# Performance work log

Hardware: AMD Instinct MI355X
Metric: run time of the kernel (lower is better)

Reference implementation:

```python
import jax, jax.numpy as jnp
import numpy as np

NEG = -1e30  # stand-in for -inf that keeps logaddexp grad-safe


def _ctc_neg_log_likelihood(predictions, labels):
    # predictions: [B, T, C] logits; labels: [B, L] int, -1 = padding.
    # tf.nn.ctc_loss(blank_index=-1) => blank class is C-1.
    B, T, C = predictions.shape
    L = labels.shape[1]
    S = 2 * L + 1
    blank = C - 1

    label_len = jnp.sum((labels != -1).astype(jnp.int32), axis=-1)  # [B]
    labels_c = jnp.where(labels < 0, 0, labels).astype(jnp.int32)

    # Extended label sequence: blank, l1, blank, l2, ..., blank  -> [B, S]
    ext = jnp.full((B, S), blank, dtype=jnp.int32)
    ext = ext.at[:, 1::2].set(labels_c)

    # s-2 transition allowed only at label positions (odd s) with ext[s] != ext[s-2]
    same = jnp.concatenate([jnp.zeros((B, 2), bool), ext[:, 2:] == ext[:, :-2]], axis=1)
    is_label_pos = (jnp.arange(S) % 2 == 1)[None, :]
    allow2 = is_label_pos & ~same  # [B, S]

    # valid extended positions per example: s < 2*label_len + 1
    valid = jnp.arange(S)[None, :] < (2 * label_len + 1)[:, None]  # [B, S]

    log_probs = jax.nn.log_softmax(predictions, axis=-1)  # [B, T, C]
    # emission log-prob for each extended-label slot: [B, T, S]
    lp_ext = jnp.take_along_axis(log_probs, jnp.broadcast_to(ext[:, None, :], (B, T, S)), axis=2)

    has_lab = label_len > 0
    alpha0 = jnp.full((B, S), NEG, dtype=log_probs.dtype)
    alpha0 = alpha0.at[:, 0].set(lp_ext[:, 0, 0])
    alpha0 = alpha0.at[:, 1].set(jnp.where(has_lab, lp_ext[:, 0, 1], NEG))
    alpha0 = jnp.where(valid, alpha0, NEG)

    def step(alpha, lp_t):
        a1 = alpha
        a2 = jnp.pad(alpha, ((0, 0), (1, 0)), constant_values=NEG)[:, :S]
        a3 = jnp.pad(alpha, ((0, 0), (2, 0)), constant_values=NEG)[:, :S]
        a3 = jnp.where(allow2, a3, NEG)
        new = jnp.logaddexp(jnp.logaddexp(a1, a2), a3) + lp_t
        new = jnp.where(valid, new, NEG)
        return new, None

    lp_rest = jnp.moveaxis(lp_ext[:, 1:], 1, 0)  # [T-1, B, S]
    alphaT, _ = jax.lax.scan(step, alpha0, lp_rest)

    idx1 = (2 * label_len)[:, None]              # final blank
    idx2 = jnp.maximum(idx1 - 1, 0)              # final label
    a_end1 = jnp.take_along_axis(alphaT, idx1, axis=1)[:, 0]
    a_end2 = jnp.take_along_axis(alphaT, idx2, axis=1)[:, 0]
    a_end2 = jnp.where(has_lab, a_end2, NEG)
    log_lik = jnp.logaddexp(a_end1, a_end2)
    return -log_lik  # [B]


def setup_inputs() -> dict:
    key = jax.random.key(0)
    k1, k2 = jax.random.split(key)
    B, T, C, L = 1024, 384, 96, 48
    labels = jax.random.randint(k1, (B, L), 0, C - 1).astype(jnp.int64)
    predictions = jax.random.normal(k2, (B, T, C), dtype=jnp.float32)
    return {"labels": labels, "predictions": predictions}


def reference(labels, predictions):
    per_example = _ctc_neg_log_likelihood(predictions, labels)
    return jnp.mean(per_example)
```

## Files before the change

kernel.cpp:

```cpp
#include <hip/hip_runtime.h>

constexpr int Tt = 384;
constexpr int Cc = 96;
constexpr int Ll = 48;
constexpr int Gg = 8;
constexpr int NG = 24;

#define L2E 1.4426950408889634f
#define LN2 0.6931471805599453f
#define LNEG (-3.0e38f)

template <int CTRL, int RM = 0xF>
__device__ __forceinline__ float dppf(float x) {
    return __int_as_float(
        __builtin_amdgcn_update_dpp(0, __float_as_int(x), CTRL, RM, 0xF, true));
}
template <int CTRL>
__device__ __forceinline__ int dppi(int x) {
    return __builtin_amdgcn_update_dpp(0, x, CTRL, 0xF, 0xF, true);
}
__device__ __forceinline__ float bcast63(float x) {
    return __int_as_float(__builtin_amdgcn_readlane(__float_as_int(x), 63));
}
__device__ __forceinline__ float wsum(float x) {
    x += dppf<0x111>(x);
    x += dppf<0x112>(x);
    x += dppf<0x114>(x);
    x += dppf<0x118>(x);
    x += dppf<0x142, 0xA>(x);
    x += dppf<0x143, 0xC>(x);
    return bcast63(x);
}
__device__ __forceinline__ float shup1(float x) { return dppf<0x138>(x); }
__device__ __forceinline__ float shdn1(float x) { return dppf<0x130>(x); }
__device__ __forceinline__ float exp2i(int d) {
    d = d < -126 ? -126 : (d > 126 ? 126 : d);
    return __int_as_float((d + 127) << 23);
}

template <bool FWD>
__device__ __forceinline__ void prod_load(const float2* __restrict__ rp2, float2* q,
                                          int g, int lane) {
#pragma unroll
    for (int j = 0; j < Gg; ++j) {
        int k = g * Gg + j;
        int t = FWD ? k : (Tt - 1 - k);
        q[j] = (lane < 48) ? rp2[(size_t)t * 48 + lane] : make_float2(-1e4f, -1e4f);
    }
}

__device__ __forceinline__ void softmax_group(const float2* q, float* pl, float* pb,
                                              int idx_h, int bitsel) {
#pragma unroll
    for (int j = 0; j < Gg; ++j) {
        float ex = __builtin_amdgcn_exp2f(q[j].x * L2E);
        float ey = __builtin_amdgcn_exp2f(q[j].y * L2E);
        float gb = __shfl(ey, 47, 64);
        float g0 = __shfl(ex, idx_h, 64);
        float g1 = __shfl(ey, idx_h, 64);
        float s  = wsum(ex + ey);
        float rZ = __builtin_amdgcn_rcpf(s);
        pl[j] = (bitsel ? g1 : g0) * rZ;
        pb[j] = gb * rZ;
    }
}

template <bool FWD>
__device__ __forceinline__ void dp_group(const float* pl, const float* pb,
                                         float allow2f, float& st_e, float& st_o,
                                         int& ls, float& f, float& a2f) {
#pragma unroll
    for (int j = 0; j < Gg; ++j) {
        if (FWD) {
            float sh = shup1(st_o);
            float t0 = st_e + st_o;
            float ne = fmaf(f, sh, st_e) * pb[j];
            float no = fmaf(a2f, sh, t0) * pl[j];
            st_e = ne; st_o = no;
        } else {
            float en = shdn1(st_e);
            float on = shdn1(st_o);
            float ne = (st_e + st_o) * pb[j];
            float no = fmaf(a2f, on, fmaf(f, en, st_o)) * pl[j];
            st_e = ne; st_o = no;
        }
    }
    float m = fmaxf(st_e, st_o);
    bool z  = (m == 0.0f);
    int eb  = (__float_as_int(m) >> 23) & 0xFF;
    eb = eb > 253 ? 253 : eb;
    float r = z ? 1.0f : __int_as_float((254 - eb) << 23);
    st_e *= r; st_o *= r;
    ls += z ? 0 : (eb - 127);
#pragma unroll
    for (int it = 0; it < 8; ++it) {
        int lsn = FWD ? dppi<0x138>(ls) : dppi<0x130>(ls);
        ls = z ? lsn : ls;
    }
    int lsn2 = FWD ? dppi<0x138>(ls) : dppi<0x130>(ls);
    f   = exp2i(lsn2 - ls);
    a2f = allow2f * f;
}

template <bool FWD>
__device__ __forceinline__ void run_half(const float2* __restrict__ rp2, int lane,
                                         int idx_h, int bitsel, float allow2f,
                                         float& st_e, float& st_o, int& ls,
                                         float& f, float& a2f) {
    float2 q0[Gg], q1[Gg];
    float plA[Gg], pbA[Gg], plB[Gg], pbB[Gg];
    prod_load<FWD>(rp2, q0, 0, lane);
    prod_load<FWD>(rp2, q1, 1, lane);
    softmax_group(q0, plA, pbA, idx_h, bitsel);
    for (int g2 = 0; g2 < NG / 2; ++g2) {
        bool more = (g2 < NG / 2 - 1);
        if (more) prod_load<FWD>(rp2, q0, 2 * g2 + 2, lane);
        softmax_group(q1, plB, pbB, idx_h, bitsel);
        dp_group<FWD>(plA, pbA, allow2f, st_e, st_o, ls, f, a2f);
        if (more) prod_load<FWD>(rp2, q1, 2 * g2 + 3, lane);
        if (more) softmax_group(q0, plA, pbA, idx_h, bitsel);
        dp_group<FWD>(plB, pbB, allow2f, st_e, st_o, ls, f, a2f);
    }
}

__global__ __launch_bounds__(64) void zero_kernel(float* o) { *o = 0.0f; }

__global__ __launch_bounds__(128) void ctc_fb(const int* __restrict__ labels,
                                              const float* __restrict__ pred,
                                              float* __restrict__ out,
                                              float invB) {
    const int b    = blockIdx.x;
    const int lane = threadIdx.x & 63;
    const int wv   = threadIdx.x >> 6;
    const float2* rp2 = (const float2*)(pred + (size_t)b * Tt * Cc);

    __shared__ float sbe[64], sbo[64];
    __shared__ int   slsb[64];

    int v = (lane < Ll) ? labels[(size_t)b * Ll + lane] : -1;
    int present = (lane < Ll) && (v != -1);
    int labv = (v < 0) ? 0 : v;
    unsigned long long pm = __ballot(present);
    int len = __popcll(pm);
    int idx_h  = labv >> 1;
    int bitsel = labv & 1;
    int lab_p = __shfl(labv, (lane - 1) & 63, 64);
    int lab_n = __shfl(labv, (lane + 1) & 63, 64);

    float st_e, st_o = 0.0f, f = 1.0f, a2f, allow2f;
    int   ls = 0;

    if (wv == 0) {
        allow2f = (lane >= 1 && labv != lab_p) ? 1.0f : 0.0f;
        st_e = (lane == 0) ? 1.0f : 0.0f;
        a2f = allow2f;
        run_half<true>(rp2, lane, idx_h, bitsel, allow2f, st_e, st_o, ls, f, a2f);
    } else {
        allow2f = (labv != lab_n) ? 1.0f : 0.0f;
        st_e = (lane == len) ? 1.0f : 0.0f;
        a2f = allow2f;
        run_half<false>(rp2, lane, idx_h, bitsel, allow2f, st_e, st_o, ls, f, a2f);
        sbe[lane]  = st_e;
        sbo[lane]  = st_o;
        slsb[lane] = ls;
    }
    __syncthreads();

    if (wv == 0) {
        float sh  = shup1(st_o);
        int   lsu = dppi<0x138>(ls);
        float fup = exp2i(lsu - ls);
        float Ae = fmaf(fup, sh, st_e);
        float Ao = fmaf(allow2f * fup, sh, st_e + st_o);
        float be = sbe[lane], bo = sbo[lane];
        float base = (float)(ls + slsb[lane]);
        float l1 = (Ae > 0.0f && be > 0.0f) ? __log2f(Ae) + __log2f(be) + base : LNEG;
        float l2 = (Ao > 0.0f && bo > 0.0f) ? __log2f(Ao) + __log2f(bo) + base : LNEG;
        float mm = fmaxf(l1, l2);
#pragma unroll
        for (int off = 32; off >= 1; off >>= 1) mm = fmaxf(mm, __shfl_xor(mm, off, 64));
        float ss = exp2f(l1 - mm) + exp2f(l2 - mm);
#pragma unroll
        for (int off = 32; off >= 1; off >>= 1) ss += __shfl_xor(ss, off, 64);
        if (lane == 0) {
            float ll = (mm + __log2f(ss)) * LN2;
            atomicAdd(out, -ll * invB);
        }
    }
}

extern "C" void kernel_launch(void* const* d_in, const int* in_sizes, int n_in,
                              void* d_out, int out_size, void* d_ws, size_t ws_size,
                              hipStream_t stream) {
    const int*   labels = (const int*)d_in[0];
    const float* pred   = (const float*)d_in[1];
    float*       out    = (float*)d_out;

    const int B = in_sizes[0] / Ll;

    hipLaunchKernelGGL(zero_kernel, dim3(1), dim3(64), 0, stream, out);
    hipLaunchKernelGGL(ctc_fb, dim3(B), dim3(128), 0, stream,
                       labels, pred, out, 1.0f / (float)B);
}
```

Baseline: 223.3 us.

## Factor softmax normalizer into separate parallel kernel and use unnormalized emissions in DP

Splits the work into two kernels. The first computes the per-example sum over time of the log partition function, using 8 waves per example so the reduction runs in parallel. The DP kernel then uses unnormalized exp(logit) emissions gathered directly at the label and blank columns, and subtracts the summed log-normalizer at the end. This takes the per-step wave-wide reduction and shuffles off the serial recurrence critical path. In exchange the predictions are read twice, a double-precision accumulation is added, and the unnormalized values may change how often the scaling mechanism has to renormalize.

```diff
diff --git a/kernel.cpp b/kernel.cpp
--- a/kernel.cpp
+++ b/kernel.cpp
@@ -38,60 +38,87 @@
     return __int_as_float((d + 127) << 23);
 }
 
+__global__ __launch_bounds__(512) void ctc_zsum(const float* __restrict__ pred,
+                                                float* __restrict__ zs,
+                                                float* __restrict__ out) {
+    const int b    = blockIdx.x;
+    const int lane = threadIdx.x & 63;
+    const int wv   = threadIdx.x >> 6;
+    const float2* rp2 = (const float2*)(pred + (size_t)b * Tt * Cc);
+    __shared__ double part[8];
+
+    if (b == 0 && threadIdx.x == 0) out[0] = 0.0f;
+
+    const int t0 = wv * 48;
+    double acc = 0.0;
+    float2 qa = (lane < 48) ? rp2[(size_t)t0 * 48 + lane] : make_float2(-1e4f, -1e4f);
+    for (int j = 0; j < 48; ++j) {
+        float2 qn = qa;
+        if (j + 1 < 48)
+            qn = (lane < 48) ? rp2[(size_t)(t0 + j + 1) * 48 + lane]
+                             : make_float2(-1e4f, -1e4f);
+        float ex = __builtin_amdgcn_exp2f(qa.x * L2E);
+        float ey = __builtin_amdgcn_exp2f(qa.y * L2E);
+        float z  = wsum(ex + ey);
+        acc += (double)__log2f(z);
+        qa = qn;
+    }
+    if (lane == 0) part[wv] = acc;
+    __syncthreads();
+    if (threadIdx.x == 0) {
+        double s = 0.0;
+#pragma unroll
+        for (int w = 0; w < 8; ++w) s += part[w];
+        zs[b] = (float)s;
+    }
+}
+
+
 template <bool FWD>
-__device__ __forceinline__ void prod_load(const float2* __restrict__ rp2, float2* q,
-                                          int g, int lane) {
+__device__ __forceinline__ void dp_load(const float* __restrict__ rp, float* ql,
+                                        float* qb, int g, int labv) {
 #pragma unroll
     for (int j = 0; j < Gg; ++j) {
         int k = g * Gg + j;
         int t = FWD ? k : (Tt - 1 - k);
-        q[j] = (lane < 48) ? rp2[(size_t)t * 48 + lane] : make_float2(-1e4f, -1e4f);
-    }
-}
-
-__device__ __forceinline__ void softmax_group(const float2* q, float* pl, float* pb,
-                                              int idx_h, int bitsel) {
-#pragma unroll
-    for (int j = 0; j < Gg; ++j) {
-        float ex = __builtin_amdgcn_exp2f(q[j].x * L2E);
-        float ey = __builtin_amdgcn_exp2f(q[j].y * L2E);
-        float gb = __shfl(ey, 47, 64);
-        float g0 = __shfl(ex, idx_h, 64);
-        float g1 = __shfl(ey, idx_h, 64);
-        float s  = wsum(ex + ey);
-        float rZ = __builtin_amdgcn_rcpf(s);
-        pl[j] = (bitsel ? g1 : g0) * rZ;
-        pb[j] = gb * rZ;
+        ql[j] = rp[t * Cc + labv];
+        qb[j] = rp[t * Cc + 95];
     }
 }
 
 template <bool FWD>
-__device__ __forceinline__ void dp_group(const float* pl, const float* pb,
+__device__ __forceinline__ void dp_group(const float* ql, const float* qb,
                                          float allow2f, float& st_e, float& st_o,
                                          int& ls, float& f, float& a2f) {
+    float el[Gg], eb[Gg];
+#pragma unroll
+    for (int j = 0; j < Gg; ++j) {
+        el[j] = __builtin_amdgcn_exp2f(ql[j] * L2E);
+        eb[j] = __builtin_amdgcn_exp2f(qb[j] * L2E);
+    }
 #pragma unroll
     for (int j = 0; j < Gg; ++j) {
         if (FWD) {
             float sh = shup1(st_o);
             float t0 = st_e + st_o;
-            float ne = fmaf(f, sh, st_e) * pb[j];
-            float no = fmaf(a2f, sh, t0) * pl[j];
+            float ne = fmaf(f, sh, st_e) * eb[j];
+            float no = fmaf(a2f, sh, t0) * el[j];
             st_e = ne; st_o = no;
         } else {
             float en = shdn1(st_e);
             float on = shdn1(st_o);
-            float ne = (st_e + st_o) * pb[j];
-            float no = fmaf(a2f, on, fmaf(f, en, st_o)) * pl[j];
+            float ne = (st_e + st_o) * eb[j];
+            float no = fmaf(a2f, on, fmaf(f, en, st_o)) * el[j];
             st_e = ne; st_o = no;
         }
     }
     float m = fmaxf(st_e, st_o);
     bool z  = (m == 0.0f);
-    int eb  = (__float_as_int(m) >> 23) & 0xFF;
-    eb = eb > 253 ? 253 : eb;
-    float r = z ? 1.0f : __int_as_float((254 - eb) << 23);
+    int eb2 = (__float_as_int(m) >> 23) & 0xFF;
+    eb2 = eb2 > 253 ? 253 : eb2;
+    float r = z ? 1.0f : __int_as_float((254 - eb2) << 23);
     st_e *= r; st_o *= r;
-    ls += z ? 0 : (eb - 127);
+    ls += z ? 0 : (eb2 - 127);
 #pragma unroll
     for (int it = 0; it < 8; ++it) {
         int lsn = FWD ? dppi<0x138>(ls) : dppi<0x130>(ls);
@@ -103,47 +130,51 @@
 }
 
 template <bool FWD>
-__device__ __forceinline__ void run_half(const float2* __restrict__ rp2, int lane,
-                                         int idx_h, int bitsel, float allow2f,
-                                         float& st_e, float& st_o, int& ls,
-                                         float& f, float& a2f) {
-    float2 q0[Gg], q1[Gg];
-    float plA[Gg], pbA[Gg], plB[Gg], pbB[Gg];
-    prod_load<FWD>(rp2, q0, 0, lane);
-    prod_load<FWD>(rp2, q1, 1, lane);
-    softmax_group(q0, plA, pbA, idx_h, bitsel);
-    for (int g2 = 0; g2 < NG / 2; ++g2) {
-        bool more = (g2 < NG / 2 - 1);
-        if (more) prod_load<FWD>(rp2, q0, 2 * g2 + 2, lane);
-        softmax_group(q1, plB, pbB, idx_h, bitsel);
-        dp_group<FWD>(plA, pbA, allow2f, st_e, st_o, ls, f, a2f);
-        if (more) prod_load<FWD>(rp2, q1, 2 * g2 + 3, lane);
-        if (more) softmax_group(q0, plA, pbA, idx_h, bitsel);
-        dp_group<FWD>(plB, pbB, allow2f, st_e, st_o, ls, f, a2f);
-    }
-}
-
-__global__ __launch_bounds__(64) void zero_kernel(float* o) { *o = 0.0f; }
-
-__global__ __launch_bounds__(128) void ctc_fb(const int* __restrict__ labels,
+__device__ __forceinline__ void run_half(const float* __restrict__ rp, int labv,
+                                         float allow2f, float& st_e, float& st_o,
+                                         int& ls, float& f, float& a2f) {
+    float qlA[Gg], qbA[Gg], qlB[Gg], qbB[Gg], qlC[Gg], qbC[Gg], qlD[Gg], qbD[Gg];
+    dp_load<FWD>(rp, qlA, qbA, 0, labv);
+    dp_load<FWD>(rp, qlB, qbB, 1, labv);
+    dp_load<FWD>(rp, qlC, qbC, 2, labv);
+    dp_load<FWD>(rp, qlD, qbD, 3, labv);
+    for (int g4 = 0; g4 < 5; ++g4) {
+        int gb = g4 * 4;
+        dp_group<FWD>(qlA, qbA, allow2f, st_e, st_o, ls, f, a2f);
+        dp_load<FWD>(rp, qlA, qbA, gb + 4, labv);
+        dp_group<FWD>(qlB, qbB, allow2f, st_e, st_o, ls, f, a2f);
+        dp_load<FWD>(rp, qlB, qbB, gb + 5, labv);
+        dp_group<FWD>(qlC, qbC, allow2f, st_e, st_o, ls, f, a2f);
+        dp_load<FWD>(rp, qlC, qbC, gb + 6, labv);
+        dp_group<FWD>(qlD, qbD, allow2f, st_e, st_o, ls, f, a2f);
+        dp_load<FWD>(rp, qlD, qbD, gb + 7, labv);
+    }
+    dp_group<FWD>(qlA, qbA, allow2f, st_e, st_o, ls, f, a2f);
+    dp_group<FWD>(qlB, qbB, allow2f, st_e, st_o, ls, f, a2f);
+    dp_group<FWD>(qlC, qbC, allow2f, st_e, st_o, ls, f, a2f);
+    dp_group<FWD>(qlD, qbD, allow2f, st_e, st_o, ls, f, a2f);
+}
+
+__global__ __launch_bounds__(128) void ctc_dp(const int* __restrict__ labels,
                                               const float* __restrict__ pred,
+                                              const float* __restrict__ zs,
                                               float* __restrict__ out,
                                               float invB) {
     const int b    = blockIdx.x;
     const int lane = threadIdx.x & 63;
     const int wv   = threadIdx.x >> 6;
-    const float2* rp2 = (const float2*)(pred + (size_t)b * Tt * Cc);
+    const float* rp = pred + (size_t)b * Tt * Cc;
 
     __shared__ float sbe[64], sbo[64];
     __shared__ int   slsb[64];
+
+    float zsb = zs[b];
 
     int v = (lane < Ll) ? labels[(size_t)b * Ll + lane] : -1;
     int present = (lane < Ll) && (v != -1);
     int labv = (v < 0) ? 0 : v;
     unsigned long long pm = __ballot(present);
     int len = __popcll(pm);
-    int idx_h  = labv >> 1;
-    int bitsel = labv & 1;
     int lab_p = __shfl(labv, (lane - 1) & 63, 64);
     int lab_n = __shfl(labv, (lane + 1) & 63, 64);
 
@@ -154,12 +185,12 @@
         allow2f = (lane >= 1 && labv != lab_p) ? 1.0f : 0.0f;
         st_e = (lane == 0) ? 1.0f : 0.0f;
         a2f = allow2f;
-        run_half<true>(rp2, lane, idx_h, bitsel, allow2f, st_e, st_o, ls, f, a2f);
+        run_half<true>(rp, labv, allow2f, st_e, st_o, ls, f, a2f);
     } else {
         allow2f = (labv != lab_n) ? 1.0f : 0.0f;
         st_e = (lane == len) ? 1.0f : 0.0f;
         a2f = allow2f;
-        run_half<false>(rp2, lane, idx_h, bitsel, allow2f, st_e, st_o, ls, f, a2f);
+        run_half<false>(rp, labv, allow2f, st_e, st_o, ls, f, a2f);
         sbe[lane]  = st_e;
         sbo[lane]  = st_o;
         slsb[lane] = ls;
@@ -183,7 +214,7 @@
 #pragma unroll
         for (int off = 32; off >= 1; off >>= 1) ss += __shfl_xor(ss, off, 64);
         if (lane == 0) {
-            float ll = (mm + __log2f(ss)) * LN2;
+            float ll = (mm + __log2f(ss) - zsb) * LN2;
             atomicAdd(out, -ll * invB);
         }
     }
@@ -195,10 +226,11 @@
     const int*   labels = (const int*)d_in[0];
     const float* pred   = (const float*)d_in[1];
     float*       out    = (float*)d_out;
+    float*       zs     = (float*)d_ws;
 
     const int B = in_sizes[0] / Ll;
 
-    hipLaunchKernelGGL(zero_kernel, dim3(1), dim3(64), 0, stream, out);
-    hipLaunchKernelGGL(ctc_fb, dim3(B), dim3(128), 0, stream,
-                       labels, pred, out, 1.0f / (float)B);
-}
+    hipLaunchKernelGGL(ctc_zsum, dim3(B), dim3(512), 0, stream, pred, zs, out);
+    hipLaunchKernelGGL(ctc_dp, dim3(B), dim3(128), 0, stream,
+                       labels, pred, zs, out, 1.0f / (float)B);
+}
```

After: 248.8 us. +11.4%, slower.
